# Kernel tuning notes

Measured on AMD Instinct MI355X. Metric: run time of the kernel, lower is better.

The kernel has to match this reference:

```python
import jax, jax.numpy as jnp
import numpy as np
from jax import lax

B, C, H, W = 4, 64, 256, 256
T, Q = 16, 0.2
C2 = 2 * C


def conv2d(x, w, b, pad):
    y = lax.conv_general_dilated(x, w, (1, 1), [(pad, pad), (pad, pad)],
                                 dimension_numbers=('NCHW', 'OIHW', 'NCHW'))
    return y + b[None, :, None, None]


def setup_inputs() -> dict:
    key = jax.random.key(0)
    ks = jax.random.split(key, 10)
    x = jax.random.normal(ks[0], (B, C, H, W), dtype=jnp.float32)
    lms = jax.random.normal(ks[1], (B, 4, H, W), dtype=jnp.float32)
    # params (kaiming-ish scale)
    W_conv = jax.random.normal(ks[2], (C2, C, 3, 3), dtype=jnp.float32) * (1.0 / np.sqrt(C * 9))
    b_conv = jnp.zeros((C2,), dtype=jnp.float32)
    W_out = jax.random.normal(ks[3], (4, C2), dtype=jnp.float32) * (1.0 / np.sqrt(C2))  # 1x1 conv as matrix
    b_out = jnp.zeros((4,), dtype=jnp.float32)
    W_aue = jax.random.normal(ks[4], (4, C2, 3, 3), dtype=jnp.float32) * (1.0 / np.sqrt(C2 * 9))
    b_aue = jnp.zeros((4,), dtype=jnp.float32)
    # T Bernoulli(1-q) channel masks, fixed for reproducibility  [T, 2C]
    masks = jax.random.bernoulli(ks[5], 1.0 - Q, (T, C2)).astype(jnp.float32)
    return {"x": x, "lms": lms, "W_conv": W_conv, "b_conv": b_conv,
            "W_out": W_out, "b_out": b_out, "W_aue": W_aue, "b_aue": b_aue,
            "masks": masks}


def reference(x, lms, W_conv, b_conv, W_out, b_out, W_aue, b_aue, masks):
    # feature extraction: 3x3 conv C -> 2C
    h = conv2d(x, W_conv, b_conv, 1)                      # [B, 2C, H, W]
    # MC-dropout samples: out(mask_t * h) == (W_out * mask_t) @ h  (1x1 conv is linear)
    Wt = W_out[None, :, :] * masks[:, None, :]            # [T, 4, 2C]
    samples = jnp.tanh(jnp.einsum('toc,bchw->tbohw', Wt, h)
                       + b_out[None, None, :, None, None]) + lms[None]  # [T, B, 4, H, W]
    mean = jnp.mean(samples, axis=0)
    EU = jnp.var(samples, axis=0, ddof=1)                 # unbiased variance over T
    AU = jax.nn.sigmoid(conv2d(h, W_aue, b_aue, 1))       # [B, 4, H, W]
    return (AU, EU, mean)
```

## Files before the change

### kernel.cpp

```cpp
#include <hip/hip_runtime.h>

#define Bsz 4
#define Cin 64
#define C2c 128
#define Hh 256
#define Ww 256
#define Tt 16
#define HW (Hh*Ww)
#define PLANE (Bsz*4*HW)

typedef __attribute__((ext_vector_type(8))) short bf16x8;
typedef __attribute__((ext_vector_type(4))) float f32x4;

#define XT_OFF  0
#define WBF_OFF 33554432
#define WTB_OFF 33701888
#define AUB_OFF 33718272

#define XP 76
#define HP 132

__device__ __forceinline__ unsigned short f2bf(float f) {
  union { float f; unsigned u; } cv; cv.f = f;
  unsigned u = cv.u;
  unsigned r = (u + 0x7fffu + ((u >> 16) & 1u)) >> 16;
  return (unsigned short)r;
}

union U8 { uint2 u2[2]; uint4 u4; bf16x8 v; };

__global__ void prep_kernel(const float* __restrict__ W_out, const float* __restrict__ masks,
                            const float* __restrict__ Wc, const float* __restrict__ W_aue,
                            unsigned short* __restrict__ Wtb, unsigned short* __restrict__ Wbf,
                            unsigned short* __restrict__ Aub) {
  int i = blockIdx.x * 256 + threadIdx.x;
  if (i < 8192) {
    int to = i >> 7, c = i & 127;
    int t = to >> 2, o = to & 3;
    Wtb[i] = f2bf(W_out[o * C2c + c] * masks[t * C2c + c]);
  } else if (i < 8192 + 73728) {
    int idx = i - 8192;
    int j = idx & 7;
    int lane = (idx >> 3) & 63;
    int nt = (idx >> 9) & 7;
    int c = idx >> 12;
    int q = lane >> 4;
    int tap = c >> 1;
    int ic = (c & 1) * 32 + q * 8 + j;
    int n = nt * 16 + (lane & 15);
    Wbf[idx] = f2bf(Wc[((size_t)n * Cin + ic) * 9 + tap]);
  } else if (i < 8192 + 73728 + 18432) {
    int idx = i - 8192 - 73728;
    int m = idx / 1152, k = idx % 1152;
    int tap = k >> 7, c = k & 127;
    float v = (m < 4) ? W_aue[((size_t)m * C2c + c) * 9 + tap] : 0.f;
    Aub[idx] = f2bf(v);
  }
}

__global__ __launch_bounds__(256) void xt_kernel(const float* __restrict__ x,
                                                 unsigned short* __restrict__ xT) {
  __shared__ unsigned short xs[64][65];
  const int tid = threadIdx.x;
  const int x0 = blockIdx.x * 64, y = blockIdx.y, bi = blockIdx.z;
  const int tx = tid & 63, ti = tid >> 6;
  #pragma unroll
  for (int i = 0; i < 16; ++i) {
    int ic = ti * 16 + i;
    float v = x[(((size_t)bi * Cin + ic) * Hh + y) * Ww + x0 + tx];
    xs[ic][tx] = f2bf(v);
  }
  __syncthreads();
  const int icg = tid & 7, xl = tid >> 3;
  #pragma unroll
  for (int rep = 0; rep < 2; ++rep) {
    int xx = xl + 32 * rep;
    unsigned short u[8];
    #pragma unroll
    for (int k = 0; k < 8; ++k) u[k] = xs[icg * 8 + k][xx];
    *(uint4*)(xT + (((size_t)bi * Hh + y) * Ww + (x0 + xx)) * Cin + icg * 8) = *(uint4*)u;
  }
}

__global__ __launch_bounds__(256, 3) void fused_kernel(
    const unsigned short* __restrict__ xT, const unsigned short* __restrict__ Wbf,
    const unsigned short* __restrict__ Wtb, const unsigned short* __restrict__ Aub,
    const float* __restrict__ bc, const float* __restrict__ b_out,
    const float* __restrict__ b_aue, const float* __restrict__ lms,
    float* __restrict__ out) {
  __shared__ unsigned short sh[192 * HP];
  const int tid = threadIdx.x;
  const int x0 = blockIdx.x * 16, y0 = blockIdx.y * 8, bi = blockIdx.z;

  for (int g = tid; g < 12 * 20 * 8; g += 256) {
    int icg = g & 7;
    int xc = (g >> 3) % 20;
    int xr = g / 160;
    int gy = y0 - 2 + xr, gx = x0 - 2 + xc;
    uint2 lo = make_uint2(0, 0), hi = make_uint2(0, 0);
    if ((unsigned)gy < Hh && (unsigned)gx < Ww) {
      uint4 v = *(const uint4*)(xT + (((size_t)bi * Hh + gy) * Ww + gx) * Cin + icg * 8);
      lo.x = v.x; lo.y = v.y; hi.x = v.z; hi.y = v.w;
    }
    int e = (xr * 20 + xc) * XP + icg * 8;
    *(uint2*)(&sh[e]) = lo;
    *(uint2*)(&sh[e + 4]) = hi;
  }
  __syncthreads();

  const int lane = tid & 63, wv = tid >> 6;
  const int n16 = lane & 15, q = lane >> 4;

  int xbase[3];
  #pragma unroll
  for (int s = 0; s < 3; ++s) {
    int px = (wv * 3 + s) * 16 + n16;
    int pr = px / 18, pc = px % 18;
    xbase[s] = (pr * 20 + pc) * XP + q * 8;
  }

  f32x4 acc[3][8];
  #pragma unroll
  for (int s = 0; s < 3; ++s)
    #pragma unroll
    for (int mt = 0; mt < 8; ++mt) acc[s][mt] = (f32x4){0.f, 0.f, 0.f, 0.f};

  #pragma unroll
  for (int c = 0; c < 18; ++c) {
    const int tap = c >> 1, ichalf = (c & 1) * 32;
    const int dy = tap / 3, dx = tap % 3;
    const int xoff = (dy * 20 + dx) * XP + ichalf;
    bf16x8 xfr[3];
    #pragma unroll
    for (int s = 0; s < 3; ++s) {
      U8 t;
      int e = xbase[s] + xoff;
      t.u2[0] = *(const uint2*)(&sh[e]);
      t.u2[1] = *(const uint2*)(&sh[e + 4]);
      xfr[s] = t.v;
    }
    #pragma unroll
    for (int mh = 0; mh < 2; ++mh) {
      bf16x8 wfr[4];
      const unsigned short* wb = Wbf + ((size_t)(c * 8 + mh * 4) * 64 + lane) * 8;
      #pragma unroll
      for (int i4 = 0; i4 < 4; ++i4)
        wfr[i4] = ((const U8*)(wb + i4 * 512))->v;
      #pragma unroll
      for (int s = 0; s < 3; ++s)
        #pragma unroll
        for (int i4 = 0; i4 < 4; ++i4)
          acc[s][mh * 4 + i4] =
            __builtin_amdgcn_mfma_f32_16x16x32_bf16(wfr[i4], xfr[s], acc[s][mh * 4 + i4], 0, 0, 0);
    }
  }
  __syncthreads();

  #pragma unroll
  for (int s = 0; s < 3; ++s) {
    const int px = (wv * 3 + s) * 16 + n16;
    const int pr = px / 18, pc = px % 18;
    const int gy = y0 - 1 + pr, gx = x0 - 1 + pc;
    const bool valid = ((unsigned)gy < Hh) && ((unsigned)gx < Ww);
    #pragma unroll
    for (int mt = 0; mt < 8; ++mt) {
      const int oc0 = mt * 16 + q * 4;
      const float4 b4 = *(const float4*)(bc + oc0);
      ushort4 o4;
      o4.x = valid ? f2bf(acc[s][mt][0] + b4.x) : (unsigned short)0;
      o4.y = valid ? f2bf(acc[s][mt][1] + b4.y) : (unsigned short)0;
      o4.z = valid ? f2bf(acc[s][mt][2] + b4.z) : (unsigned short)0;
      o4.w = valid ? f2bf(acc[s][mt][3] + b4.w) : (unsigned short)0;
      *(ushort4*)(&sh[px * HP + oc0]) = o4;
    }
  }
  __syncthreads();

  f32x4 accG[2][4];
  f32x4 accA[2];
  #pragma unroll
  for (int nt = 0; nt < 2; ++nt) {
    accA[nt] = (f32x4){0.f, 0.f, 0.f, 0.f};
    #pragma unroll
    for (int mt = 0; mt < 4; ++mt) accG[nt][mt] = (f32x4){0.f, 0.f, 0.f, 0.f};
  }

  #pragma unroll
  for (int kc = 0; kc < 4; ++kc) {
    bf16x8 afr[4];
    #pragma unroll
    for (int mt = 0; mt < 4; ++mt)
      afr[mt] = ((const U8*)(Wtb + (size_t)(mt * 16 + n16) * C2c + kc * 32 + q * 8))->v;
    #pragma unroll
    for (int nt = 0; nt < 2; ++nt) {
      int e = (((wv * 2 + nt) + 1) * 18 + n16 + 1) * HP + kc * 32 + q * 8;
      U8 b;
      b.u2[0] = *(const uint2*)(&sh[e]);
      b.u2[1] = *(const uint2*)(&sh[e + 4]);
      #pragma unroll
      for (int mt = 0; mt < 4; ++mt)
        accG[nt][mt] = __builtin_amdgcn_mfma_f32_16x16x32_bf16(afr[mt], b.v, accG[nt][mt], 0, 0, 0);
    }
  }

  #pragma unroll
  for (int kc = 0; kc < 36; ++kc) {
    const int tap = kc >> 2, co = (kc & 3) * 32;
    const int dy = tap / 3, dx = tap % 3;
    bf16x8 afr = ((const U8*)(Aub + (size_t)n16 * 1152 + kc * 32 + q * 8))->v;
    #pragma unroll
    for (int nt = 0; nt < 2; ++nt) {
      int e = ((wv * 2 + nt + dy) * 18 + n16 + dx) * HP + co + q * 8;
      U8 b;
      b.u2[0] = *(const uint2*)(&sh[e]);
      b.u2[1] = *(const uint2*)(&sh[e + 4]);
      accA[nt] = __builtin_amdgcn_mfma_f32_16x16x32_bf16(afr, b.v, accA[nt], 0, 0, 0);
    }
  }

  const float b0 = b_out[0], b1 = b_out[1], b2 = b_out[2], b3 = b_out[3];
  const float ba = b_aue[q];
  const int px = x0 + n16;
  #pragma unroll
  for (int nt = 0; nt < 2; ++nt) {
    const int y = y0 + wv * 2 + nt;
    float th[4][4];
    #pragma unroll
    for (int mt = 0; mt < 4; ++mt) {
      #pragma unroll
      for (int r = 0; r < 4; ++r) {
        float bo = (r == 0) ? b0 : (r == 1) ? b1 : (r == 2) ? b2 : b3;
        float v = accG[nt][mt][r] + bo;
        float e = __expf(2.f * v);
        th[mt][r] = 1.f - 2.f / (e + 1.f);
      }
    }
    float mean_r[4], eu_r[4];
    #pragma unroll
    for (int r = 0; r < 4; ++r) {
      float s = th[0][r] + th[1][r] + th[2][r] + th[3][r];
      s += __shfl_xor(s, 16);
      s += __shfl_xor(s, 32);
      float m = s * (1.f / 16.f);
      float d0 = th[0][r] - m, d1 = th[1][r] - m, d2 = th[2][r] - m, d3 = th[3][r] - m;
      float vs = d0 * d0 + d1 * d1 + d2 * d2 + d3 * d3;
      vs += __shfl_xor(vs, 16);
      vs += __shfl_xor(vs, 32);
      mean_r[r] = m;
      eu_r[r] = vs * (1.f / 15.f);
    }
    float au_r[4];
    #pragma unroll
    for (int r = 0; r < 4; ++r) au_r[r] = __shfl(accA[nt][r], n16);

    float m_q  = (q == 0) ? mean_r[0] : (q == 1) ? mean_r[1] : (q == 2) ? mean_r[2] : mean_r[3];
    float eu_q = (q == 0) ? eu_r[0]   : (q == 1) ? eu_r[1]   : (q == 2) ? eu_r[2]   : eu_r[3];
    float au_q = (q == 0) ? au_r[0]   : (q == 1) ? au_r[1]   : (q == 2) ? au_r[2]   : au_r[3];
    au_q = 1.f / (1.f + __expf(-(au_q + ba)));
    size_t oidx = ((size_t)(bi * 4 + q)) * HW + (size_t)y * Ww + px;
    float lm = lms[oidx];
    out[oidx] = au_q;
    out[PLANE + oidx] = eu_q;
    out[2 * (size_t)PLANE + oidx] = m_q + lm;
  }
}

extern "C" void kernel_launch(void* const* d_in, const int* in_sizes, int n_in,
                              void* d_out, int out_size, void* d_ws, size_t ws_size,
                              hipStream_t stream) {
  const float* x      = (const float*)d_in[0];
  const float* lms    = (const float*)d_in[1];
  const float* W_conv = (const float*)d_in[2];
  const float* b_conv = (const float*)d_in[3];
  const float* W_out  = (const float*)d_in[4];
  const float* b_out  = (const float*)d_in[5];
  const float* W_aue  = (const float*)d_in[6];
  const float* b_aue  = (const float*)d_in[7];
  const float* masks  = (const float*)d_in[8];
  float* out = (float*)d_out;

  char* ws = (char*)d_ws;
  unsigned short* xT  = (unsigned short*)(ws + XT_OFF);
  unsigned short* Wbf = (unsigned short*)(ws + WBF_OFF);
  unsigned short* Wtb = (unsigned short*)(ws + WTB_OFF);
  unsigned short* Aub = (unsigned short*)(ws + AUB_OFF);

  prep_kernel<<<dim3(392), dim3(256), 0, stream>>>(W_out, masks, W_conv, W_aue, Wtb, Wbf, Aub);
  xt_kernel<<<dim3(4, 256, 4), dim3(256), 0, stream>>>(x, xT);
  fused_kernel<<<dim3(16, 32, 4), dim3(256), 0, stream>>>(xT, Wbf, Wtb, Aub, b_conv,
                                                          b_out, b_aue, lms, out);
}
```

Before: 223.7 us.

## Fuse NCHW-to-bf16 transpose into conv kernel and pad h tile for 128-bit LDS reads

Removes the separate xt_kernel and its intermediate bf16 NHWC buffer. The fused kernel now reads fp32 x straight from NCHW, converts it to bf16 and scatters it into the shared-memory halo tile, which saves a launch and a full round trip of x through global memory. The h tile pitch goes from 132 to 136 so B-fragment reads can be single 128-bit LDS loads. In exchange, each of the 512 tiles per batch re-reads its halo in fp32 with 64-byte row segments. The per-element scalar LDS stores may bank-conflict, and the new pitch changes the bank pattern of the h reads.

```diff
diff --git a/kernel.cpp b/kernel.cpp
--- a/kernel.cpp
+++ b/kernel.cpp
@@ -12,13 +12,12 @@
 typedef __attribute__((ext_vector_type(8))) short bf16x8;
 typedef __attribute__((ext_vector_type(4))) float f32x4;
 
-#define XT_OFF  0
-#define WBF_OFF 33554432
-#define WTB_OFF 33701888
-#define AUB_OFF 33718272
+#define WBF_OFF 0
+#define WTB_OFF 147456
+#define AUB_OFF 163840
 
 #define XP 76
-#define HP 132
+#define HP 136
 
 __device__ __forceinline__ unsigned short f2bf(float f) {
   union { float f; unsigned u; } cv; cv.f = f;
@@ -58,32 +57,8 @@
   }
 }
 
-__global__ __launch_bounds__(256) void xt_kernel(const float* __restrict__ x,
-                                                 unsigned short* __restrict__ xT) {
-  __shared__ unsigned short xs[64][65];
-  const int tid = threadIdx.x;
-  const int x0 = blockIdx.x * 64, y = blockIdx.y, bi = blockIdx.z;
-  const int tx = tid & 63, ti = tid >> 6;
-  #pragma unroll
-  for (int i = 0; i < 16; ++i) {
-    int ic = ti * 16 + i;
-    float v = x[(((size_t)bi * Cin + ic) * Hh + y) * Ww + x0 + tx];
-    xs[ic][tx] = f2bf(v);
-  }
-  __syncthreads();
-  const int icg = tid & 7, xl = tid >> 3;
-  #pragma unroll
-  for (int rep = 0; rep < 2; ++rep) {
-    int xx = xl + 32 * rep;
-    unsigned short u[8];
-    #pragma unroll
-    for (int k = 0; k < 8; ++k) u[k] = xs[icg * 8 + k][xx];
-    *(uint4*)(xT + (((size_t)bi * Hh + y) * Ww + (x0 + xx)) * Cin + icg * 8) = *(uint4*)u;
-  }
-}
-
 __global__ __launch_bounds__(256, 3) void fused_kernel(
-    const unsigned short* __restrict__ xT, const unsigned short* __restrict__ Wbf,
+    const float* __restrict__ x, const unsigned short* __restrict__ Wbf,
     const unsigned short* __restrict__ Wtb, const unsigned short* __restrict__ Aub,
     const float* __restrict__ bc, const float* __restrict__ b_out,
     const float* __restrict__ b_aue, const float* __restrict__ lms,
@@ -92,19 +67,23 @@
   const int tid = threadIdx.x;
   const int x0 = blockIdx.x * 16, y0 = blockIdx.y * 8, bi = blockIdx.z;
 
-  for (int g = tid; g < 12 * 20 * 8; g += 256) {
-    int icg = g & 7;
-    int xc = (g >> 3) % 20;
-    int xr = g / 160;
-    int gy = y0 - 2 + xr, gx = x0 - 2 + xc;
-    uint2 lo = make_uint2(0, 0), hi = make_uint2(0, 0);
-    if ((unsigned)gy < Hh && (unsigned)gx < Ww) {
-      uint4 v = *(const uint4*)(xT + (((size_t)bi * Hh + gy) * Ww + gx) * Cin + icg * 8);
-      lo.x = v.x; lo.y = v.y; hi.x = v.z; hi.y = v.w;
-    }
-    int e = (xr * 20 + xc) * XP + icg * 8;
-    *(uint2*)(&sh[e]) = lo;
-    *(uint2*)(&sh[e + 4]) = hi;
+  {
+    const int ic = tid & 63;
+    const int xr0 = tid >> 6;
+    #pragma unroll
+    for (int rr = 0; rr < 3; ++rr) {
+      const int xr = xr0 * 3 + rr;
+      const int gy = y0 - 2 + xr;
+      const bool rowok = (unsigned)gy < Hh;
+      const float* src = x + (((size_t)bi * Cin + ic) * Hh + gy) * Ww;
+      const int lbase = (xr * 20) * XP + ic;
+      #pragma unroll
+      for (int xc = 0; xc < 20; ++xc) {
+        const int gx = x0 - 2 + xc;
+        float v = (rowok && (unsigned)gx < Ww) ? src[gx] : 0.f;
+        sh[lbase + xc * XP] = f2bf(v);
+      }
+    }
   }
   __syncthreads();
 
@@ -194,9 +173,7 @@
     #pragma unroll
     for (int nt = 0; nt < 2; ++nt) {
       int e = (((wv * 2 + nt) + 1) * 18 + n16 + 1) * HP + kc * 32 + q * 8;
-      U8 b;
-      b.u2[0] = *(const uint2*)(&sh[e]);
-      b.u2[1] = *(const uint2*)(&sh[e + 4]);
+      U8 b; b.u4 = *(const uint4*)(&sh[e]);
       #pragma unroll
       for (int mt = 0; mt < 4; ++mt)
         accG[nt][mt] = __builtin_amdgcn_mfma_f32_16x16x32_bf16(afr[mt], b.v, accG[nt][mt], 0, 0, 0);
@@ -211,9 +188,7 @@
     #pragma unroll
     for (int nt = 0; nt < 2; ++nt) {
       int e = ((wv * 2 + nt + dy) * 18 + n16 + dx) * HP + co + q * 8;
-      U8 b;
-      b.u2[0] = *(const uint2*)(&sh[e]);
-      b.u2[1] = *(const uint2*)(&sh[e + 4]);
+      U8 b; b.u4 = *(const uint4*)(&sh[e]);
       accA[nt] = __builtin_amdgcn_mfma_f32_16x16x32_bf16(afr, b.v, accA[nt], 0, 0, 0);
     }
   }
@@ -280,13 +255,11 @@
   float* out = (float*)d_out;
 
   char* ws = (char*)d_ws;
-  unsigned short* xT  = (unsigned short*)(ws + XT_OFF);
   unsigned short* Wbf = (unsigned short*)(ws + WBF_OFF);
   unsigned short* Wtb = (unsigned short*)(ws + WTB_OFF);
   unsigned short* Aub = (unsigned short*)(ws + AUB_OFF);
 
   prep_kernel<<<dim3(392), dim3(256), 0, stream>>>(W_out, masks, W_conv, W_aue, Wtb, Wbf, Aub);
-  xt_kernel<<<dim3(4, 256, 4), dim3(256), 0, stream>>>(x, xT);
-  fused_kernel<<<dim3(16, 32, 4), dim3(256), 0, stream>>>(xT, Wbf, Wtb, Aub, b_conv,
+  fused_kernel<<<dim3(16, 32, 4), dim3(256), 0, stream>>>(x, Wbf, Wtb, Aub, b_conv,
                                                           b_out, b_aue, lms, out);
 }
```

New measurement: 332.3 us. 1.49x slower.

## Split conv MFMA work by output-channel half per wave and use 16-byte LDS loads

Applied to the files above, without the earlier changes.

The first conv stage is repartitioned so each wave handles one half of the output channels across six pixel tiles, instead of all eight channel tiles across three pixel tiles. Each wave now loads four weight fragments per step instead of eight, which cuts global/L2 weight traffic per wave, though it reads more activation fragments from LDS. LDS row pitches change to 72 and 136 shorts so rows stay 16-byte aligned, allowing single 128-bit LDS loads and stores in place of paired 64-bit ones. The new pitches may change bank-conflict behaviour.

```diff
diff --git a/kernel.cpp b/kernel.cpp
--- a/kernel.cpp
+++ b/kernel.cpp
@@ -17,8 +17,8 @@
 #define WTB_OFF 33701888
 #define AUB_OFF 33718272
 
-#define XP 76
-#define HP 132
+#define XP 72
+#define HP 136
 
 __device__ __forceinline__ unsigned short f2bf(float f) {
   union { float f; unsigned u; } cv; cv.f = f;
@@ -97,80 +97,67 @@
     int xc = (g >> 3) % 20;
     int xr = g / 160;
     int gy = y0 - 2 + xr, gx = x0 - 2 + xc;
-    uint2 lo = make_uint2(0, 0), hi = make_uint2(0, 0);
-    if ((unsigned)gy < Hh && (unsigned)gx < Ww) {
-      uint4 v = *(const uint4*)(xT + (((size_t)bi * Hh + gy) * Ww + gx) * Cin + icg * 8);
-      lo.x = v.x; lo.y = v.y; hi.x = v.z; hi.y = v.w;
-    }
-    int e = (xr * 20 + xc) * XP + icg * 8;
-    *(uint2*)(&sh[e]) = lo;
-    *(uint2*)(&sh[e + 4]) = hi;
+    uint4 v = make_uint4(0, 0, 0, 0);
+    if ((unsigned)gy < Hh && (unsigned)gx < Ww)
+      v = *(const uint4*)(xT + (((size_t)bi * Hh + gy) * Ww + gx) * Cin + icg * 8);
+    *(uint4*)(&sh[(xr * 20 + xc) * XP + icg * 8]) = v;
   }
   __syncthreads();
 
   const int lane = tid & 63, wv = tid >> 6;
   const int n16 = lane & 15, q = lane >> 4;
-
-  int xbase[3];
-  #pragma unroll
-  for (int s = 0; s < 3; ++s) {
-    int px = (wv * 3 + s) * 16 + n16;
+  const int mh = wv & 1;
+  const int s6 = wv >> 1;
+
+  int xbase[6];
+  #pragma unroll
+  for (int ss = 0; ss < 6; ++ss) {
+    int px = (s6 * 6 + ss) * 16 + n16;
     int pr = px / 18, pc = px % 18;
-    xbase[s] = (pr * 20 + pc) * XP + q * 8;
-  }
-
-  f32x4 acc[3][8];
-  #pragma unroll
-  for (int s = 0; s < 3; ++s)
-    #pragma unroll
-    for (int mt = 0; mt < 8; ++mt) acc[s][mt] = (f32x4){0.f, 0.f, 0.f, 0.f};
+    xbase[ss] = (pr * 20 + pc) * XP + q * 8;
+  }
+
+  f32x4 acc[6][4];
+  #pragma unroll
+  for (int ss = 0; ss < 6; ++ss)
+    #pragma unroll
+    for (int i4 = 0; i4 < 4; ++i4) acc[ss][i4] = (f32x4){0.f, 0.f, 0.f, 0.f};
 
   #pragma unroll
   for (int c = 0; c < 18; ++c) {
     const int tap = c >> 1, ichalf = (c & 1) * 32;
     const int dy = tap / 3, dx = tap % 3;
     const int xoff = (dy * 20 + dx) * XP + ichalf;
-    bf16x8 xfr[3];
-    #pragma unroll
-    for (int s = 0; s < 3; ++s) {
-      U8 t;
-      int e = xbase[s] + xoff;
-      t.u2[0] = *(const uint2*)(&sh[e]);
-      t.u2[1] = *(const uint2*)(&sh[e + 4]);
-      xfr[s] = t.v;
-    }
-    #pragma unroll
-    for (int mh = 0; mh < 2; ++mh) {
-      bf16x8 wfr[4];
-      const unsigned short* wb = Wbf + ((size_t)(c * 8 + mh * 4) * 64 + lane) * 8;
+    bf16x8 wfr[4];
+    const unsigned short* wb = Wbf + ((size_t)(c * 8 + mh * 4) * 64 + lane) * 8;
+    #pragma unroll
+    for (int i4 = 0; i4 < 4; ++i4)
+      wfr[i4] = ((const U8*)(wb + i4 * 512))->v;
+    #pragma unroll
+    for (int ss = 0; ss < 6; ++ss) {
+      U8 b; b.u4 = *(const uint4*)(&sh[xbase[ss] + xoff]);
       #pragma unroll
       for (int i4 = 0; i4 < 4; ++i4)
-        wfr[i4] = ((const U8*)(wb + i4 * 512))->v;
-      #pragma unroll
-      for (int s = 0; s < 3; ++s)
-        #pragma unroll
-        for (int i4 = 0; i4 < 4; ++i4)
-          acc[s][mh * 4 + i4] =
-            __builtin_amdgcn_mfma_f32_16x16x32_bf16(wfr[i4], xfr[s], acc[s][mh * 4 + i4], 0, 0, 0);
-    }
-  }
-  __syncthreads();
-
-  #pragma unroll
-  for (int s = 0; s < 3; ++s) {
-    const int px = (wv * 3 + s) * 16 + n16;
+        acc[ss][i4] = __builtin_amdgcn_mfma_f32_16x16x32_bf16(wfr[i4], b.v, acc[ss][i4], 0, 0, 0);
+    }
+  }
+  __syncthreads();
+
+  #pragma unroll
+  for (int ss = 0; ss < 6; ++ss) {
+    const int px = (s6 * 6 + ss) * 16 + n16;
     const int pr = px / 18, pc = px % 18;
     const int gy = y0 - 1 + pr, gx = x0 - 1 + pc;
     const bool valid = ((unsigned)gy < Hh) && ((unsigned)gx < Ww);
     #pragma unroll
-    for (int mt = 0; mt < 8; ++mt) {
-      const int oc0 = mt * 16 + q * 4;
+    for (int i4 = 0; i4 < 4; ++i4) {
+      const int oc0 = (mh * 4 + i4) * 16 + q * 4;
       const float4 b4 = *(const float4*)(bc + oc0);
       ushort4 o4;
-      o4.x = valid ? f2bf(acc[s][mt][0] + b4.x) : (unsigned short)0;
-      o4.y = valid ? f2bf(acc[s][mt][1] + b4.y) : (unsigned short)0;
-      o4.z = valid ? f2bf(acc[s][mt][2] + b4.z) : (unsigned short)0;
-      o4.w = valid ? f2bf(acc[s][mt][3] + b4.w) : (unsigned short)0;
+      o4.x = valid ? f2bf(acc[ss][i4][0] + b4.x) : (unsigned short)0;
+      o4.y = valid ? f2bf(acc[ss][i4][1] + b4.y) : (unsigned short)0;
+      o4.z = valid ? f2bf(acc[ss][i4][2] + b4.z) : (unsigned short)0;
+      o4.w = valid ? f2bf(acc[ss][i4][3] + b4.w) : (unsigned short)0;
       *(ushort4*)(&sh[px * HP + oc0]) = o4;
     }
   }
@@ -194,9 +181,7 @@
     #pragma unroll
     for (int nt = 0; nt < 2; ++nt) {
       int e = (((wv * 2 + nt) + 1) * 18 + n16 + 1) * HP + kc * 32 + q * 8;
-      U8 b;
-      b.u2[0] = *(const uint2*)(&sh[e]);
-      b.u2[1] = *(const uint2*)(&sh[e + 4]);
+      U8 b; b.u4 = *(const uint4*)(&sh[e]);
       #pragma unroll
       for (int mt = 0; mt < 4; ++mt)
         accG[nt][mt] = __builtin_amdgcn_mfma_f32_16x16x32_bf16(afr[mt], b.v, accG[nt][mt], 0, 0, 0);
@@ -211,9 +196,7 @@
     #pragma unroll
     for (int nt = 0; nt < 2; ++nt) {
       int e = ((wv * 2 + nt + dy) * 18 + n16 + dx) * HP + co + q * 8;
-      U8 b;
-      b.u2[0] = *(const uint2*)(&sh[e]);
-      b.u2[1] = *(const uint2*)(&sh[e + 4]);
+      U8 b; b.u4 = *(const uint4*)(&sh[e]);
       accA[nt] = __builtin_amdgcn_mfma_f32_16x16x32_bf16(afr, b.v, accA[nt], 0, 0, 0);
     }
   }
```

Result: no change. 227.1 us (+1.5%).
